# Optimization experiments

Hardware: AMD Instinct MI355X
Metric: run time of the kernel (lower is better)

Reference implementation:

```python
import jax, jax.numpy as jnp
import numpy as np

NUM_HEADS = 16
HEAD_DIM = 64
ROT_DIM = HEAD_DIM // 2  # RotaryEmbedding(dim=head_dim/2) rotates first 32 dims only
THETA = 10000.0


def _rope(x):
    # x: [b, h, l, d]; interleaved (lucidrains) rotary on first ROT_DIM dims.
    L = x.shape[-2]
    inv_freq = 1.0 / (THETA ** (jnp.arange(0, ROT_DIM, 2, dtype=jnp.float32) / ROT_DIM))  # [ROT_DIM/2]
    ang = jnp.arange(L, dtype=jnp.float32)[:, None] * inv_freq[None, :]  # [l, ROT_DIM/2]
    ang = jnp.repeat(ang, 2, axis=-1)  # [l, ROT_DIM] (each freq repeated for the pair)
    cos, sin = jnp.cos(ang), jnp.sin(ang)
    x_rot, x_pass = x[..., :ROT_DIM], x[..., ROT_DIM:]
    x1 = x_rot[..., 0::2]
    x2 = x_rot[..., 1::2]
    rot_half = jnp.stack([-x2, x1], axis=-1).reshape(x_rot.shape)  # rotate_half, interleaved
    x_rot = x_rot * cos + rot_half * sin
    return jnp.concatenate([x_rot, x_pass], axis=-1)


def setup_inputs() -> dict:
    key = jax.random.key(0)
    ks = jax.random.split(key, 7)
    B, L, E = 2, 2048, 1024
    s = 1.0 / np.sqrt(E)
    return {
        "query": jax.random.normal(ks[0], (B, L, E), jnp.float32),
        "key": jax.random.normal(ks[1], (B, L, E), jnp.float32),
        "value": jax.random.normal(ks[2], (B, L, E), jnp.float32),
        "Wq": jax.random.normal(ks[3], (E, E), jnp.float32) * s,
        "Wk": jax.random.normal(ks[4], (E, E), jnp.float32) * s,
        "Wv": jax.random.normal(ks[5], (E, E), jnp.float32) * s,
        "Wo": jax.random.normal(ks[6], (E, E), jnp.float32) * s,
        "bo": jnp.zeros((E,), jnp.float32),
    }


def reference(query, key, value, Wq, Wk, Wv, Wo, bo):
    B, L, E = query.shape
    H, D = NUM_HEADS, HEAD_DIM
    scaling = D ** (-0.5)

    def split_heads(x):
        return x.reshape(B, L, H, D).transpose(0, 2, 1, 3)  # b h l d

    q = split_heads(query @ Wq.T)
    k = split_heads(key @ Wk.T)
    v = split_heads(value @ Wv.T)
    q = _rope(q)
    k = _rope(k)
    # NOTE: source divides by scaling (multiplies by sqrt(D)) -- faithful to original.
    attn_weight = jnp.einsum('bhid,bhjd->bhij', q, k) / scaling
    # NOTE: softmax over dim=-2 (query axis), as in the original code.
    attn_weight = jax.nn.softmax(attn_weight, axis=-2)
    attn = jnp.einsum('bhij,bhjd->bhid', attn_weight, v)
    attn = attn.transpose(0, 2, 1, 3).reshape(B, L, E)
    out = attn @ Wo.T + bo
    return out, attn_weight
```

## Files before the change

kernel.cpp:

```cpp
#include <hip/hip_runtime.h>
#include <cmath>

typedef __bf16 bf16;
typedef __attribute__((ext_vector_type(4))) __bf16 bf16x4;
typedef __attribute__((ext_vector_type(8))) __bf16 bf16x8;
typedef __attribute__((ext_vector_type(4))) float f32x4;

#define MFMA16(a, b, c) __builtin_amdgcn_mfma_f32_16x16x32_bf16((a), (b), (c), 0, 0, 0)
#define SETPRIO1 __builtin_amdgcn_s_setprio(1)
#define SETPRIO0 __builtin_amdgcn_s_setprio(0)
#define WAITV_BAR(N) asm volatile("s_waitcnt vmcnt(" #N ")\n\ts_barrier" ::: "memory")
#define WAITL_BAR    asm volatile("s_waitcnt lgkmcnt(0)\n\ts_barrier" ::: "memory")

static __device__ __forceinline__ void gload16(const bf16* g, bf16* l)
{
  __builtin_amdgcn_global_load_lds((const __attribute__((address_space(1))) void*)g,
                                   (__attribute__((address_space(3))) void*)l, 16, 0, 0);
}

static __device__ __forceinline__ void split4(const float4 v, bf16x4& h, bf16x4& l)
{
  h[0] = (bf16)v.x; l[0] = (bf16)(v.x - (float)h[0]);
  h[1] = (bf16)v.y; l[1] = (bf16)(v.y - (float)h[1]);
  h[2] = (bf16)v.z; l[2] = (bf16)(v.z - (float)h[2]);
  h[3] = (bf16)v.w; l[3] = (bf16)(v.w - (float)h[3]);
}

__global__ __launch_bounds__(256) void conv_kernel(
    const float* __restrict__ query, const float* __restrict__ key, const float* __restrict__ value,
    const float* __restrict__ Wq, const float* __restrict__ Wk, const float* __restrict__ Wv,
    const float* __restrict__ Wo,
    bf16* __restrict__ qh, bf16* __restrict__ ql, bf16* __restrict__ kh, bf16* __restrict__ kl,
    bf16* __restrict__ wqh, bf16* __restrict__ wql, bf16* __restrict__ wkh, bf16* __restrict__ wkl,
    bf16* __restrict__ vb, bf16* __restrict__ wvb, bf16* __restrict__ wob)
{
  const int i = blockIdx.x * 256 + threadIdx.x;
  const float* src;
  bf16 *dh, *dl;
  int e;
  if (i < 1048576)      { src = query; dh = qh; dl = ql; e = i; }
  else if (i < 2097152) { src = key;   dh = kh; dl = kl; e = i - 1048576; }
  else if (i < 3145728) { src = value; dh = vb; dl = nullptr; e = i - 2097152; }
  else {
    const int w = i - 3145728;
    const int which = w >> 18;
    e = w & 262143;
    src = (which == 0) ? Wq : (which == 1) ? Wk : (which == 2) ? Wv : Wo;
    dh  = (which == 0) ? wqh : (which == 1) ? wkh : (which == 2) ? wvb : wob;
    dl  = (which == 0) ? wql : (which == 1) ? wkl : nullptr;
  }
  const float4 v = ((const float4*)src)[e];
  bf16x4 h, l;
  split4(v, h, l);
  *(bf16x4*)(dh + (size_t)e * 4) = h;
  if (dl) *(bf16x4*)(dl + (size_t)e * 4) = l;
}

__global__ __launch_bounds__(256) void projqk_kernel(
    const bf16* __restrict__ qh, const bf16* __restrict__ ql,
    const bf16* __restrict__ kh, const bf16* __restrict__ kl,
    const bf16* __restrict__ wqh, const bf16* __restrict__ wql,
    const bf16* __restrict__ wkh, const bf16* __restrict__ wkl,
    bf16* __restrict__ Qh_g, bf16* __restrict__ Ql_g,
    bf16* __restrict__ Kh_g, bf16* __restrict__ Kl_g)
{
  const int which = blockIdx.y;
  const bf16* ta[4];
  ta[0] = which ? kh : qh;   ta[1] = which ? kl : ql;
  ta[2] = which ? wkh : wqh; ta[3] = which ? wkl : wql;
  bf16* oh = which ? Kh_g : Qh_g;
  bf16* ol = which ? Kl_g : Ql_g;
  const float oscale = which ? 8.0f : 1.0f;

  __shared__ __align__(16) bf16 sm[2][4][4096];
  const int tid = threadIdx.x, lane = tid & 63, w = tid >> 6;
  const int wm = w >> 1, wn = w & 1;
  const int fr = lane & 15, fg = lane >> 4;
  const int bm = blockIdx.x >> 3, bn = blockIdx.x & 7;
  const int rb[4] = {bm * 128, bm * 128, bn * 128, bn * 128};
  const int lrow = lane >> 2, lcol = (lane & 3) * 8;

  auto stage = [&](int buf, int kt) {
#pragma unroll
    for (int tl = 0; tl < 4; ++tl)
#pragma unroll
      for (int q = 0; q < 2; ++q) {
        const int r = (q * 4 + w) * 16 + lrow;
        gload16(ta[tl] + (size_t)(rb[tl] + r) * 1024 + kt * 32 + lcol,
                &sm[buf][tl][(q * 4 + w) * 512]);
      }
  };

  f32x4 acc[4][4] = {};
  stage(0, 0);
  for (int kt = 0; kt < 32; ++kt) {
    const int cur = kt & 1;
    if (kt < 31) { stage(cur ^ 1, kt + 1); WAITV_BAR(8); }
    else         { WAITV_BAR(0); }
    bf16x8 afh[4], afl[4], bfh[4], bfl[4];
#pragma unroll
    for (int m = 0; m < 4; ++m) {
      afh[m] = *(bf16x8*)&sm[cur][0][(wm * 64 + m * 16 + fr) * 32 + fg * 8];
      afl[m] = *(bf16x8*)&sm[cur][1][(wm * 64 + m * 16 + fr) * 32 + fg * 8];
    }
#pragma unroll
    for (int n = 0; n < 4; ++n) {
      bfh[n] = *(bf16x8*)&sm[cur][2][(wn * 64 + n * 16 + fr) * 32 + fg * 8];
      bfl[n] = *(bf16x8*)&sm[cur][3][(wn * 64 + n * 16 + fr) * 32 + fg * 8];
    }
    SETPRIO1;
#pragma unroll
    for (int m = 0; m < 4; ++m)
#pragma unroll
      for (int n = 0; n < 4; ++n) {
        acc[m][n] = MFMA16(afh[m], bfh[n], acc[m][n]);
        acc[m][n] = MFMA16(afh[m], bfl[n], acc[m][n]);
        acc[m][n] = MFMA16(afl[m], bfh[n], acc[m][n]);
      }
    SETPRIO0;
    WAITL_BAR;
  }
#pragma unroll
  for (int n = 0; n < 4; ++n) {
    const int d = n * 16 + fr;
    const bool rot = (n < 2);
    const float invf = rot ? exp2f((float)(d >> 1) * (-0.83048202372184059f)) : 0.0f;
    const int odd = d & 1;
    const int col = bn * 128 + wn * 64 + n * 16 + fr;
#pragma unroll
    for (int m = 0; m < 4; ++m)
#pragma unroll
      for (int r4 = 0; r4 < 4; ++r4) {
        const int row = bm * 128 + wm * 64 + m * 16 + fg * 4 + r4;
        float x = acc[m][n][r4];
        const float p = __shfl_xor(x, 1);
        if (rot) {
          float sn, cs;
          sincosf((float)(row & 2047) * invf, &sn, &cs);
          x = odd ? x * cs + p * sn : x * cs - p * sn;
        }
        x *= oscale;
        const bf16 hv = (bf16)x;
        oh[(size_t)row * 1024 + col] = hv;
        ol[(size_t)row * 1024 + col] = (bf16)(x - (float)hv);
      }
  }
}

__global__ __launch_bounds__(256) void projv_kernel(const bf16* __restrict__ vb,
                                                    const bf16* __restrict__ wvb,
                                                    bf16* __restrict__ Vt_g)
{
  __shared__ __align__(16) bf16 sm[2][2][4096];
  const int tid = threadIdx.x, lane = tid & 63, w = tid >> 6;
  const int wm = w >> 1, wn = w & 1;
  const int fr = lane & 15, fg = lane >> 4;
  const int bm = blockIdx.x >> 3, bn = blockIdx.x & 7;
  const int lrow = lane >> 2, lcol = (lane & 3) * 8;

  auto stage = [&](int buf, int kt) {
#pragma unroll
    for (int q = 0; q < 2; ++q) {
      const int r = (q * 4 + w) * 16 + lrow;
      gload16(vb  + (size_t)(bm * 128 + r) * 1024 + kt * 32 + lcol, &sm[buf][0][(q * 4 + w) * 512]);
      gload16(wvb + (size_t)(bn * 128 + r) * 1024 + kt * 32 + lcol, &sm[buf][1][(q * 4 + w) * 512]);
    }
  };

  f32x4 acc[4][4] = {};
  stage(0, 0);
  for (int kt = 0; kt < 32; ++kt) {
    const int cur = kt & 1;
    if (kt < 31) { stage(cur ^ 1, kt + 1); WAITV_BAR(4); }
    else         { WAITV_BAR(0); }
    bf16x8 af[4], bf[4];
#pragma unroll
    for (int m = 0; m < 4; ++m) af[m] = *(bf16x8*)&sm[cur][0][(wm * 64 + m * 16 + fr) * 32 + fg * 8];
#pragma unroll
    for (int n = 0; n < 4; ++n) bf[n] = *(bf16x8*)&sm[cur][1][(wn * 64 + n * 16 + fr) * 32 + fg * 8];
    SETPRIO1;
#pragma unroll
    for (int m = 0; m < 4; ++m)
#pragma unroll
      for (int n = 0; n < 4; ++n) acc[m][n] = MFMA16(af[m], bf[n], acc[m][n]);
    SETPRIO0;
    WAITL_BAR;
  }
#pragma unroll
  for (int m = 0; m < 4; ++m) {
    const int row0 = bm * 128 + wm * 64 + m * 16 + fg * 4;
    const int b = row0 >> 11, l0 = row0 & 2047;
#pragma unroll
    for (int n = 0; n < 4; ++n) {
      const int col = bn * 128 + wn * 64 + n * 16 + fr;
      const int h = col >> 6, d = col & 63;
      bf16x4 pk;
#pragma unroll
      for (int j = 0; j < 4; ++j) pk[j] = (bf16)acc[m][n][j];
      *(bf16x4*)(Vt_g + ((size_t)((b * 16 + h) * 64 + d)) * 2048 + l0) = pk;
    }
  }
}

__global__ __launch_bounds__(256) void out_kernel(const bf16* __restrict__ attnb,
                                                  const bf16* __restrict__ wob,
                                                  const float* __restrict__ bo,
                                                  float* __restrict__ out)
{
  __shared__ __align__(16) bf16 sm[2][2][4096];
  const int tid = threadIdx.x, lane = tid & 63, w = tid >> 6;
  const int wm = w >> 1, wn = w & 1;
  const int fr = lane & 15, fg = lane >> 4;
  const int bm = blockIdx.x >> 3, bn = blockIdx.x & 7;
  const int lrow = lane >> 2, lcol = (lane & 3) * 8;

  auto stage = [&](int buf, int kt) {
#pragma unroll
    for (int q = 0; q < 2; ++q) {
      const int r = (q * 4 + w) * 16 + lrow;
      gload16(attnb + (size_t)(bm * 128 + r) * 1024 + kt * 32 + lcol, &sm[buf][0][(q * 4 + w) * 512]);
      gload16(wob   + (size_t)(bn * 128 + r) * 1024 + kt * 32 + lcol, &sm[buf][1][(q * 4 + w) * 512]);
    }
  };

  f32x4 acc[4][4] = {};
  stage(0, 0);
  for (int kt = 0; kt < 32; ++kt) {
    const int cur = kt & 1;
    if (kt < 31) { stage(cur ^ 1, kt + 1); WAITV_BAR(4); }
    else         { WAITV_BAR(0); }
    bf16x8 af[4], bf[4];
#pragma unroll
    for (int m = 0; m < 4; ++m) af[m] = *(bf16x8*)&sm[cur][0][(wm * 64 + m * 16 + fr) * 32 + fg * 8];
#pragma unroll
    for (int n = 0; n < 4; ++n) bf[n] = *(bf16x8*)&sm[cur][1][(wn * 64 + n * 16 + fr) * 32 + fg * 8];
    SETPRIO1;
#pragma unroll
    for (int m = 0; m < 4; ++m)
#pragma unroll
      for (int n = 0; n < 4; ++n) acc[m][n] = MFMA16(af[m], bf[n], acc[m][n]);
    SETPRIO0;
    WAITL_BAR;
  }
#pragma unroll
  for (int m = 0; m < 4; ++m)
#pragma unroll
    for (int n = 0; n < 4; ++n) {
      const int col = bn * 128 + wn * 64 + n * 16 + fr;
      const float bv = bo[col];
#pragma unroll
      for (int r4 = 0; r4 < 4; ++r4) {
        const int row = bm * 128 + wm * 64 + m * 16 + fg * 4 + r4;
        out[(size_t)row * 1024 + col] = acc[m][n][r4] + bv;
      }
    }
}

__global__ __launch_bounds__(512) void stats_kernel(const bf16* __restrict__ Qh_g, const bf16* __restrict__ Ql_g,
                                                    const bf16* __restrict__ Kh_g, const bf16* __restrict__ Kl_g,
                                                    float* __restrict__ colmax, float* __restrict__ colsum)
{
  __shared__ __align__(16) bf16 smh[2][8192], sml[2][8192];
  const int swz = (blockIdx.x & 7) * 64 + (blockIdx.x >> 3);
  const int bh = swz >> 4, jb = swz & 15;
  const int b = bh >> 4, h = bh & 15;
  const int t = threadIdx.x, lane = t & 63, w = t >> 6;
  const int fr = lane & 15, fg = lane >> 4;
  const int lr = lane >> 3, lc = lane & 7;

  auto stageQ = [&](int buf, int it) {
#pragma unroll
    for (int q = 0; q < 2; ++q) {
      const int r = (q * 8 + w) * 8 + lr;
      const size_t g = (size_t)(b * 2048 + it * 128 + r) * 1024 + h * 64 + ((lc ^ (r & 7)) * 8);
      gload16(Qh_g + g, &smh[buf][(q * 8 + w) * 512]);
      gload16(Ql_g + g, &sml[buf][(q * 8 + w) * 512]);
    }
  };

#pragma unroll
  for (int q = 0; q < 2; ++q) {
    const int r = (q * 8 + w) * 8 + lr;
    const size_t g = (size_t)(b * 2048 + jb * 128 + r) * 1024 + h * 64 + ((lc ^ (r & 7)) * 8);
    gload16(Kh_g + g, &smh[1][(q * 8 + w) * 512]);
    gload16(Kl_g + g, &sml[1][(q * 8 + w) * 512]);
  }
  stageQ(0, 0);
  WAITV_BAR(4);
  bf16x8 kfh[2], kfl[2];
#pragma unroll
  for (int ks = 0; ks < 2; ++ks) {
    const int rr = w * 16 + fr;
    const int cc = (ks * 32 + fg * 8) ^ ((rr & 7) << 3);
    kfh[ks] = *(bf16x8*)&smh[1][rr * 64 + cc];
    kfl[ks] = *(bf16x8*)&sml[1][rr * 64 + cc];
  }
  WAITL_BAR;

  float rm[4] = {-1e30f, -1e30f, -1e30f, -1e30f};
  float rs[4] = {0.f, 0.f, 0.f, 0.f};
  for (int it = 0; it < 16; ++it) {
    const int cur = it & 1;
    if (it < 15) { stageQ(cur ^ 1, it + 1); WAITV_BAR(4); }
    else         { WAITV_BAR(0); }
    f32x4 acc[8] = {};
    SETPRIO1;
#pragma unroll
    for (int ks = 0; ks < 2; ++ks)
#pragma unroll
      for (int n = 0; n < 8; ++n) {
        const int rr = n * 16 + fr;
        const int cc = (ks * 32 + fg * 8) ^ ((rr & 7) << 3);
        const bf16x8 qf = *(bf16x8*)&smh[cur][rr * 64 + cc];
        const bf16x8 lf = *(bf16x8*)&sml[cur][rr * 64 + cc];
        acc[n] = MFMA16(kfh[ks], qf, acc[n]);
        acc[n] = MFMA16(kfh[ks], lf, acc[n]);
        acc[n] = MFMA16(kfl[ks], qf, acc[n]);
      }
    SETPRIO0;
    float tm[4];
#pragma unroll
    for (int r4 = 0; r4 < 4; ++r4) {
      float m = acc[0][r4];
#pragma unroll
      for (int n = 1; n < 8; ++n) m = fmaxf(m, acc[n][r4]);
      tm[r4] = m;
    }
#pragma unroll
    for (int off = 1; off < 16; off <<= 1)
#pragma unroll
      for (int r4 = 0; r4 < 4; ++r4) tm[r4] = fmaxf(tm[r4], __shfl_xor(tm[r4], off));
#pragma unroll
    for (int r4 = 0; r4 < 4; ++r4) {
      const float mn = fmaxf(rm[r4], tm[r4]);
      float ts = 0.f;
#pragma unroll
      for (int n = 0; n < 8; ++n) ts += __expf(acc[n][r4] - mn);
#pragma unroll
      for (int off = 1; off < 16; off <<= 1) ts += __shfl_xor(ts, off);
      rs[r4] = rs[r4] * __expf(rm[r4] - mn) + ts;
      rm[r4] = mn;
    }
    WAITL_BAR;
  }
  if (fr == 0) {
#pragma unroll
    for (int r4 = 0; r4 < 4; ++r4) {
      const int j = jb * 128 + w * 16 + fg * 4 + r4;
      colmax[bh * 2048 + j] = rm[r4];
      colsum[bh * 2048 + j] = rs[r4];
    }
  }
}

__global__ __launch_bounds__(256) void attn_kernel(const bf16* __restrict__ Qh_g, const bf16* __restrict__ Ql_g,
                                                   const bf16* __restrict__ Kh_g, const bf16* __restrict__ Kl_g,
                                                   const bf16* __restrict__ Vt_g,
                                                   const float* __restrict__ colmax, const float* __restrict__ colsum,
                                                   float* __restrict__ P, bf16* __restrict__ attnb)
{
  __shared__ __align__(16) unsigned char smem[46080];
  bf16(*Kh)[72] = (bf16(*)[72])smem;
  bf16(*Kl)[72] = (bf16(*)[72])(smem + 9216);
  bf16(*Vt)[72] = (bf16(*)[72])(smem + 18432);
  bf16(*Pb)[72] = (bf16(*)[72])(smem + 27648);
  bf16(*Qh)[72] = (bf16(*)[72])smem;
  bf16(*Ql)[72] = (bf16(*)[72])(smem + 18432);

  const int swz = (blockIdx.x & 7) * 64 + (blockIdx.x >> 3);
  const int bh = swz >> 4, ib = swz & 15;
  const int b = bh >> 4, h = bh & 15;
  const int t = threadIdx.x, lane = t & 63, w = t >> 6;
  const int fr = lane & 15, fg = lane >> 4;

#pragma unroll
  for (int q = 0; q < 4; ++q) {
    const int u = q * 256 + t, r = u >> 3, c8 = (u & 7) * 8;
    const size_t g = (size_t)(b * 2048 + ib * 128 + r) * 1024 + h * 64 + c8;
    *(bf16x8*)&Qh[r][c8] = *(const bf16x8*)(Qh_g + g);
    *(bf16x8*)&Ql[r][c8] = *(const bf16x8*)(Ql_g + g);
  }
  WAITL_BAR;
  bf16x8 qfh[2][2], qfl[2][2];
#pragma unroll
  for (int mf = 0; mf < 2; ++mf)
#pragma unroll
    for (int ks = 0; ks < 2; ++ks) {
      qfh[mf][ks] = *(bf16x8*)&Qh[w * 32 + mf * 16 + fr][ks * 32 + fg * 8];
      qfl[mf][ks] = *(bf16x8*)&Ql[w * 32 + mf * 16 + fr][ks * 32 + fg * 8];
    }

  bf16x8 rKh[2], rKl[2], rV[2];
  auto loadT = [&](int jt1) {
#pragma unroll
    for (int q = 0; q < 2; ++q) {
      const int u = q * 256 + t, r = u >> 3, c8 = (u & 7) * 8;
      const size_t g = (size_t)(b * 2048 + jt1 * 64 + r) * 1024 + h * 64 + c8;
      rKh[q] = *(const bf16x8*)(Kh_g + g);
      rKl[q] = *(const bf16x8*)(Kl_g + g);
      rV[q]  = *(const bf16x8*)(Vt_g + (size_t)(bh * 64 + r) * 2048 + jt1 * 64 + c8);
    }
  };
  auto writeT = [&]() {
#pragma unroll
    for (int q = 0; q < 2; ++q) {
      const int u = q * 256 + t, r = u >> 3, c8 = (u & 7) * 8;
      *(bf16x8*)&Kh[r][c8] = rKh[q];
      *(bf16x8*)&Kl[r][c8] = rKl[q];
      *(bf16x8*)&Vt[r][c8] = rV[q];
    }
  };

  loadT(0);
  WAITL_BAR;
  writeT();
  WAITL_BAR;

  f32x4 oacc[2][4] = {};
  for (int jt = 0; jt < 32; ++jt) {
    if (jt < 31) loadT(jt + 1);
    f32x4 s[2][4] = {};
    SETPRIO1;
#pragma unroll
    for (int ks = 0; ks < 2; ++ks)
#pragma unroll
      for (int nj = 0; nj < 4; ++nj) {
        const bf16x8 khf = *(bf16x8*)&Kh[nj * 16 + fr][ks * 32 + fg * 8];
        const bf16x8 klf = *(bf16x8*)&Kl[nj * 16 + fr][ks * 32 + fg * 8];
#pragma unroll
        for (int mf = 0; mf < 2; ++mf) {
          s[mf][nj] = MFMA16(qfh[mf][ks], khf, s[mf][nj]);
          s[mf][nj] = MFMA16(qfh[mf][ks], klf, s[mf][nj]);
          s[mf][nj] = MFMA16(qfl[mf][ks], khf, s[mf][nj]);
        }
      }
    SETPRIO0;
#pragma unroll
    for (int nj = 0; nj < 4; ++nj) {
      const int jg = jt * 64 + nj * 16 + fr;
      const float cm = colmax[bh * 2048 + jg];
      const float rcs = 1.0f / colsum[bh * 2048 + jg];
#pragma unroll
      for (int mf = 0; mf < 2; ++mf)
#pragma unroll
        for (int r4 = 0; r4 < 4; ++r4) {
          const int il = w * 32 + mf * 16 + fg * 4 + r4;
          const float pv = __expf(s[mf][nj][r4] - cm) * rcs;
          P[(size_t)(bh * 2048 + ib * 128 + il) * 2048 + jg] = pv;
          Pb[il][nj * 16 + fr] = (bf16)pv;
        }
    }
    WAITL_BAR;
    SETPRIO1;
#pragma unroll
    for (int ks = 0; ks < 2; ++ks) {
      bf16x8 pa[2];
#pragma unroll
      for (int mf = 0; mf < 2; ++mf) pa[mf] = *(bf16x8*)&Pb[w * 32 + mf * 16 + fr][ks * 32 + fg * 8];
#pragma unroll
      for (int nd = 0; nd < 4; ++nd) {
        const bf16x8 vbf = *(bf16x8*)&Vt[nd * 16 + fr][ks * 32 + fg * 8];
#pragma unroll
        for (int mf = 0; mf < 2; ++mf) oacc[mf][nd] = MFMA16(pa[mf], vbf, oacc[mf][nd]);
      }
    }
    SETPRIO0;
    WAITL_BAR;
    if (jt < 31) { writeT(); WAITL_BAR; }
  }
#pragma unroll
  for (int mf = 0; mf < 2; ++mf)
#pragma unroll
    for (int nd = 0; nd < 4; ++nd)
#pragma unroll
      for (int r4 = 0; r4 < 4; ++r4) {
        const int il = ib * 128 + w * 32 + mf * 16 + fg * 4 + r4;
        attnb[(size_t)(b * 2048 + il) * 1024 + h * 64 + nd * 16 + fr] = (bf16)oacc[mf][nd][r4];
      }
}

extern "C" void kernel_launch(void* const* d_in, const int* in_sizes, int n_in,
                              void* d_out, int out_size, void* d_ws, size_t ws_size,
                              hipStream_t stream)
{
  const float* query = (const float*)d_in[0];
  const float* key   = (const float*)d_in[1];
  const float* value = (const float*)d_in[2];
  const float* Wq    = (const float*)d_in[3];
  const float* Wk    = (const float*)d_in[4];
  const float* Wv    = (const float*)d_in[5];
  const float* Wo    = (const float*)d_in[6];
  const float* bo    = (const float*)d_in[7];

  float* out = (float*)d_out;
  float* P   = out + 4194304;

  bf16* qh  = (bf16*)(P + 0);
  bf16* ql  = (bf16*)(P + 2097152);
  bf16* kh  = (bf16*)(P + 4194304);
  bf16* kl  = (bf16*)(P + 6291456);
  bf16* wqh = (bf16*)(P + 8388608);
  bf16* wql = (bf16*)(P + 8912896);
  bf16* wkh = (bf16*)(P + 9437184);
  bf16* wkl = (bf16*)(P + 9961472);
  bf16* vb  = (bf16*)(P + 10485760);
  bf16* wvb = (bf16*)(P + 12582912);

  float* ws   = (float*)d_ws;
  bf16* Qh_g  = (bf16*)(ws + 0);
  bf16* Ql_g  = (bf16*)(ws + 2097152);
  bf16* Kh_g  = (bf16*)(ws + 4194304);
  bf16* Kl_g  = (bf16*)(ws + 6291456);
  bf16* Vt_g  = (bf16*)(ws + 8388608);
  bf16* attnb = (bf16*)(ws + 10485760);
  bf16* wob   = (bf16*)(ws + 12582912);
  float* cmax = ws + 13107200;
  float* csum = ws + 13172736;

  conv_kernel<<<16384, 256, 0, stream>>>(query, key, value, Wq, Wk, Wv, Wo,
                                         qh, ql, kh, kl, wqh, wql, wkh, wkl, vb, wvb, wob);
  projqk_kernel<<<dim3(256, 2), 256, 0, stream>>>(qh, ql, kh, kl, wqh, wql, wkh, wkl,
                                                  Qh_g, Ql_g, Kh_g, Kl_g);
  projv_kernel<<<256, 256, 0, stream>>>(vb, wvb, Vt_g);
  stats_kernel<<<512, 512, 0, stream>>>(Qh_g, Ql_g, Kh_g, Kl_g, cmax, csum);
  attn_kernel<<<512, 256, 0, stream>>>(Qh_g, Ql_g, Kh_g, Kl_g, Vt_g, cmax, csum, P, attnb);
  out_kernel<<<256, 256, 0, stream>>>(attnb, wob, bo, out);
}
```

Measured before the change: 389.2 us.

## Transpose attention MFMA outputs for vectorized P stores and fold log2e into K

Swaps the MFMA operand order in the attention kernel so each lane holds four consecutive key columns. That lets the probability matrix be written as nontemporal 16-byte stores, the column stats be read as vectors, and the bf16 output be written as 4-wide stores. The log2e factor is folded into the K projection scale so exp2f replaces __expf, and the column-sum reciprocal is precomputed in the stats kernel. K and V shared-memory refills are split so the K write overlaps the PV MFMAs, which also removes one barrier per tile. The main cost targeted is the scattered scalar writes of the large fp32 attention-weight output.

```diff
diff --git a/kernel.cpp b/kernel.cpp
--- a/kernel.cpp
+++ b/kernel.cpp
@@ -11,6 +11,8 @@
 #define SETPRIO0 __builtin_amdgcn_s_setprio(0)
 #define WAITV_BAR(N) asm volatile("s_waitcnt vmcnt(" #N ")\n\ts_barrier" ::: "memory")
 #define WAITL_BAR    asm volatile("s_waitcnt lgkmcnt(0)\n\ts_barrier" ::: "memory")
+
+#define LOG2E 1.4426950408889634f
 
 static __device__ __forceinline__ void gload16(const bf16* g, bf16* l)
 {
@@ -70,7 +72,7 @@
   ta[2] = which ? wkh : wqh; ta[3] = which ? wkl : wql;
   bf16* oh = which ? Kh_g : Qh_g;
   bf16* ol = which ? Kl_g : Ql_g;
-  const float oscale = which ? 8.0f : 1.0f;
+  const float oscale = which ? 8.0f * LOG2E : 1.0f;
 
   __shared__ __align__(16) bf16 sm[2][4][4096];
   const int tid = threadIdx.x, lane = tid & 63, w = tid >> 6;
@@ -258,7 +260,7 @@
 
 __global__ __launch_bounds__(512) void stats_kernel(const bf16* __restrict__ Qh_g, const bf16* __restrict__ Ql_g,
                                                     const bf16* __restrict__ Kh_g, const bf16* __restrict__ Kl_g,
-                                                    float* __restrict__ colmax, float* __restrict__ colsum)
+                                                    float* __restrict__ colmax, float* __restrict__ csuminv)
 {
   __shared__ __align__(16) bf16 smh[2][8192], sml[2][8192];
   const int swz = (blockIdx.x & 7) * 64 + (blockIdx.x >> 3);
@@ -335,10 +337,10 @@
       const float mn = fmaxf(rm[r4], tm[r4]);
       float ts = 0.f;
 #pragma unroll
-      for (int n = 0; n < 8; ++n) ts += __expf(acc[n][r4] - mn);
+      for (int n = 0; n < 8; ++n) ts += exp2f(acc[n][r4] - mn);
 #pragma unroll
       for (int off = 1; off < 16; off <<= 1) ts += __shfl_xor(ts, off);
-      rs[r4] = rs[r4] * __expf(rm[r4] - mn) + ts;
+      rs[r4] = rs[r4] * exp2f(rm[r4] - mn) + ts;
       rm[r4] = mn;
     }
     WAITL_BAR;
@@ -348,7 +350,7 @@
     for (int r4 = 0; r4 < 4; ++r4) {
       const int j = jb * 128 + w * 16 + fg * 4 + r4;
       colmax[bh * 2048 + j] = rm[r4];
-      colsum[bh * 2048 + j] = rs[r4];
+      csuminv[bh * 2048 + j] = 1.0f / rs[r4];
     }
   }
 }
@@ -356,7 +358,7 @@
 __global__ __launch_bounds__(256) void attn_kernel(const bf16* __restrict__ Qh_g, const bf16* __restrict__ Ql_g,
                                                    const bf16* __restrict__ Kh_g, const bf16* __restrict__ Kl_g,
                                                    const bf16* __restrict__ Vt_g,
-                                                   const float* __restrict__ colmax, const float* __restrict__ colsum,
+                                                   const float* __restrict__ colmax, const float* __restrict__ csuminv,
                                                    float* __restrict__ P, bf16* __restrict__ attnb)
 {
   __shared__ __align__(16) unsigned char smem[46080];
@@ -401,19 +403,25 @@
       rV[q]  = *(const bf16x8*)(Vt_g + (size_t)(bh * 64 + r) * 2048 + jt1 * 64 + c8);
     }
   };
-  auto writeT = [&]() {
+  auto writeK = [&]() {
 #pragma unroll
     for (int q = 0; q < 2; ++q) {
       const int u = q * 256 + t, r = u >> 3, c8 = (u & 7) * 8;
       *(bf16x8*)&Kh[r][c8] = rKh[q];
       *(bf16x8*)&Kl[r][c8] = rKl[q];
+    }
+  };
+  auto writeV = [&]() {
+#pragma unroll
+    for (int q = 0; q < 2; ++q) {
+      const int u = q * 256 + t, r = u >> 3, c8 = (u & 7) * 8;
       *(bf16x8*)&Vt[r][c8] = rV[q];
     }
   };
 
   loadT(0);
   WAITL_BAR;
-  writeT();
+  writeK(); writeV();
   WAITL_BAR;
 
   f32x4 oacc[2][4] = {};
@@ -429,28 +437,33 @@
         const bf16x8 klf = *(bf16x8*)&Kl[nj * 16 + fr][ks * 32 + fg * 8];
 #pragma unroll
         for (int mf = 0; mf < 2; ++mf) {
-          s[mf][nj] = MFMA16(qfh[mf][ks], khf, s[mf][nj]);
-          s[mf][nj] = MFMA16(qfh[mf][ks], klf, s[mf][nj]);
-          s[mf][nj] = MFMA16(qfl[mf][ks], khf, s[mf][nj]);
+          s[mf][nj] = MFMA16(khf, qfh[mf][ks], s[mf][nj]);
+          s[mf][nj] = MFMA16(klf, qfh[mf][ks], s[mf][nj]);
+          s[mf][nj] = MFMA16(khf, qfl[mf][ks], s[mf][nj]);
         }
       }
     SETPRIO0;
 #pragma unroll
     for (int nj = 0; nj < 4; ++nj) {
-      const int jg = jt * 64 + nj * 16 + fr;
-      const float cm = colmax[bh * 2048 + jg];
-      const float rcs = 1.0f / colsum[bh * 2048 + jg];
-#pragma unroll
-      for (int mf = 0; mf < 2; ++mf)
-#pragma unroll
-        for (int r4 = 0; r4 < 4; ++r4) {
-          const int il = w * 32 + mf * 16 + fg * 4 + r4;
-          const float pv = __expf(s[mf][nj][r4] - cm) * rcs;
-          P[(size_t)(bh * 2048 + ib * 128 + il) * 2048 + jg] = pv;
-          Pb[il][nj * 16 + fr] = (bf16)pv;
-        }
+      const int jb4 = jt * 64 + nj * 16 + fg * 4;
+      const f32x4 cmv = *(const f32x4*)(colmax + bh * 2048 + jb4);
+      const f32x4 rcv = *(const f32x4*)(csuminv + bh * 2048 + jb4);
+#pragma unroll
+      for (int mf = 0; mf < 2; ++mf) {
+        const int ig = ib * 128 + w * 32 + mf * 16 + fr;
+        f32x4 pv;
+        pv[0] = exp2f(s[mf][nj][0] - cmv[0]) * rcv[0];
+        pv[1] = exp2f(s[mf][nj][1] - cmv[1]) * rcv[1];
+        pv[2] = exp2f(s[mf][nj][2] - cmv[2]) * rcv[2];
+        pv[3] = exp2f(s[mf][nj][3] - cmv[3]) * rcv[3];
+        __builtin_nontemporal_store(pv, (f32x4*)(P + (size_t)(bh * 2048 + ig) * 2048 + jb4));
+        bf16x4 pb4;
+        pb4[0] = (bf16)pv[0]; pb4[1] = (bf16)pv[1]; pb4[2] = (bf16)pv[2]; pb4[3] = (bf16)pv[3];
+        *(bf16x4*)&Pb[w * 32 + mf * 16 + fr][nj * 16 + fg * 4] = pb4;
+      }
     }
     WAITL_BAR;
+    if (jt < 31) writeK();
     SETPRIO1;
 #pragma unroll
     for (int ks = 0; ks < 2; ++ks) {
@@ -461,22 +474,24 @@
       for (int nd = 0; nd < 4; ++nd) {
         const bf16x8 vbf = *(bf16x8*)&Vt[nd * 16 + fr][ks * 32 + fg * 8];
 #pragma unroll
-        for (int mf = 0; mf < 2; ++mf) oacc[mf][nd] = MFMA16(pa[mf], vbf, oacc[mf][nd]);
+        for (int mf = 0; mf < 2; ++mf) oacc[mf][nd] = MFMA16(vbf, pa[mf], oacc[mf][nd]);
       }
     }
     SETPRIO0;
     WAITL_BAR;
-    if (jt < 31) { writeT(); WAITL_BAR; }
-  }
-#pragma unroll
-  for (int mf = 0; mf < 2; ++mf)
-#pragma unroll
-    for (int nd = 0; nd < 4; ++nd)
-#pragma unroll
-      for (int r4 = 0; r4 < 4; ++r4) {
-        const int il = ib * 128 + w * 32 + mf * 16 + fg * 4 + r4;
-        attnb[(size_t)(b * 2048 + il) * 1024 + h * 64 + nd * 16 + fr] = (bf16)oacc[mf][nd][r4];
-      }
+    if (jt < 31) writeV();
+  }
+#pragma unroll
+  for (int mf = 0; mf < 2; ++mf) {
+    const int ig = ib * 128 + w * 32 + mf * 16 + fr;
+#pragma unroll
+    for (int nd = 0; nd < 4; ++nd) {
+      bf16x4 o4;
+#pragma unroll
+      for (int r4 = 0; r4 < 4; ++r4) o4[r4] = (bf16)oacc[mf][nd][r4];
+      *(bf16x4*)(attnb + (size_t)(b * 2048 + ig) * 1024 + h * 64 + nd * 16 + fg * 4) = o4;
+    }
+  }
 }
 
 extern "C" void kernel_launch(void* const* d_in, const int* in_sizes, int n_in,
@@ -515,14 +530,14 @@
   bf16* attnb = (bf16*)(ws + 10485760);
   bf16* wob   = (bf16*)(ws + 12582912);
   float* cmax = ws + 13107200;
-  float* csum = ws + 13172736;
+  float* csui = ws + 13172736;
 
   conv_kernel<<<16384, 256, 0, stream>>>(query, key, value, Wq, Wk, Wv, Wo,
                                          qh, ql, kh, kl, wqh, wql, wkh, wkl, vb, wvb, wob);
   projqk_kernel<<<dim3(256, 2), 256, 0, stream>>>(qh, ql, kh, kl, wqh, wql, wkh, wkl,
                                                   Qh_g, Ql_g, Kh_g, Kl_g);
   projv_kernel<<<256, 256, 0, stream>>>(vb, wvb, Vt_g);
-  stats_kernel<<<512, 512, 0, stream>>>(Qh_g, Ql_g, Kh_g, Kl_g, cmax, csum);
-  attn_kernel<<<512, 256, 0, stream>>>(Qh_g, Ql_g, Kh_g, Kl_g, Vt_g, cmax, csum, P, attnb);
+  stats_kernel<<<512, 512, 0, stream>>>(Qh_g, Ql_g, Kh_g, Kl_g, cmax, csui);
+  attn_kernel<<<512, 256, 0, stream>>>(Qh_g, Ql_g, Kh_g, Kl_g, Vt_g, cmax, csui, P, attnb);
   out_kernel<<<256, 256, 0, stream>>>(attnb, wob, bo, out);
 }
```

Measured after the change: 403.1 us. 3.6% more time.
